# Performance work log

Hardware: AMD Instinct MI355X
Metric: run time of the kernel (lower is better)

Reference implementation:

```python
import jax, jax.numpy as jnp
import numpy as np
from jax import lax


def setup_inputs() -> dict:
    key = jax.random.key(0)
    k1, k2, k3, k4 = jax.random.split(key, 4)
    N, D, B, R, EF = 100000, 256, 64, 32, 32
    storage = jax.random.normal(k1, (N, D), dtype=jnp.float32)
    query = jax.random.normal(k2, (B, D), dtype=jnp.float32)
    graph = jax.random.randint(k3, (N, R), 0, N, dtype=jnp.int32)      # fixed-degree NSW adjacency
    initial = jax.random.randint(k4, (B, EF), 0, N, dtype=jnp.int32)   # random entry points (entry())
    return {"query": query, "storage": storage, "graph": graph,
            "initial": initial, "k": 10, "ef_search": EF}


def reference(query, storage, graph, initial, k, ef_search):
    """Batched greedy best-first NSW search (ef_search fixed expansion steps)."""
    N = storage.shape[0]
    INF = jnp.float32(1e30)

    def sqdist(q, ids):
        diff = storage[ids] - q            # [R, D] gather
        return jnp.sum(diff * diff, axis=-1)

    def search_one(q, init):
        cd = sqdist(q, init)                               # candidate distances [EF]
        visited = jnp.zeros((N,), jnp.bool_).at[init].set(True)
        expanded = jnp.zeros((N,), jnp.bool_)

        def step(state, _):
            cid, cd, visited, expanded = state
            # pick closest unexpanded candidate
            pickd = jnp.where(expanded[cid], INF, cd)
            j = jnp.argmin(pickd)
            u = cid[j]
            expanded = expanded.at[u].set(True)
            # expand neighbors of u
            nbrs = graph[u]                                # [R]
            fresh = ~visited[nbrs]
            nd = jnp.where(fresh, sqdist(q, nbrs), INF)    # skip already-visited
            visited = visited.at[nbrs].set(True)
            # merge candidate pool, keep ef_search best
            all_ids = jnp.concatenate([cid, nbrs])
            all_d = jnp.concatenate([cd, nd])
            negd, idx = lax.top_k(-all_d, ef_search)
            return (all_ids[idx], -negd, visited, expanded), None

        (cid, cd, _, _), _ = lax.scan(step, (init, cd, visited, expanded),
                                      None, length=ef_search)
        negk, idx = lax.top_k(-cd, k)
        return cid[idx], -negk

    topk_ids, topk_dists = jax.vmap(search_one)(query, initial)
    return topk_ids, topk_dists
```

## Files before the change

kernel.cpp:

```cpp
#include <hip/hip_runtime.h>


#define DIMS   256
#define RDEG   32
#define EFPOOL 32
#define KOUT   10
#define NWORDS 3125
#define INF_D  1e30f

__global__ __launch_bounds__(64, 1) void nsw_wave_kernel(
    const float* __restrict__ query,
    const float* __restrict__ storage,
    const int*   __restrict__ graph,
    const int*   __restrict__ initial,
    float*       __restrict__ out,
    int B)
{
    __shared__ unsigned int visited[NWORDS];
    __shared__ unsigned int expanded[NWORDS];
    __shared__ float4 qsh[DIMS / 4];
    __shared__ unsigned long long keys[64];
    __shared__ float sc_d[EFPOOL];
    __shared__ int   sc_id[EFPOOL];

    const int l    = threadIdx.x;
    const int b    = blockIdx.x;
    const int nb   = l & 31;
    const int half = l >> 5;

    for (int i = l; i < NWORDS; i += 64) { visited[i] = 0u; expanded[i] = 0u; }

    qsh[l] = reinterpret_cast<const float4*>(query + (size_t)b * DIMS)[l];

    float pool_d  = INF_D;
    int   pool_id = 0;
    int   u;

    auto merge_pick = [&](float nd, int nbid) {
        float ed  = half ? nd   : pool_d;
        int   eid = half ? nbid : pool_id;
        unsigned long long key =
            ((unsigned long long)__float_as_uint(ed) << 6) | (unsigned)l;
        keys[l] = key;
        int rank = 0;
        #pragma unroll
        for (int j = 0; j < 64; ++j)
            rank += (keys[j] < key) ? 1 : 0;
        if (rank < EFPOOL) { sc_d[rank] = ed; sc_id[rank] = eid; }
        pool_d  = sc_d[nb];
        pool_id = sc_id[nb];
        bool unexp = !((expanded[pool_id >> 5] >> (pool_id & 31)) & 1u);
        unsigned long long m = __ballot(unexp && (l < 32));
        int slot = (m == 0ull) ? 0 : (__ffsll((unsigned long long)m) - 1);
        u = sc_id[slot];
        if (l == 0) expanded[u >> 5] |= (1u << (u & 31));
    };

    {
        int nbid = initial[b * EFPOOL + nb];
        const float4* sp = reinterpret_cast<const float4*>(storage + (size_t)nbid * DIMS) + half * 32;
        float4 r[32];
        #pragma unroll
        for (int j = 0; j < 32; ++j) r[j] = sp[j];
        if (l < 32) atomicOr(&visited[nbid >> 5], 1u << (nbid & 31));
        float a0 = 0.f, a1 = 0.f, a2 = 0.f, a3 = 0.f;
        #pragma unroll
        for (int j = 0; j < 32; ++j) {
            float4 q = qsh[half * 32 + j];
            float d0 = r[j].x - q.x; a0 = fmaf(d0, d0, a0);
            float d1 = r[j].y - q.y; a1 = fmaf(d1, d1, a1);
            float d2 = r[j].z - q.z; a2 = fmaf(d2, d2, a2);
            float d3 = r[j].w - q.w; a3 = fmaf(d3, d3, a3);
        }
        float part = (a0 + a1) + (a2 + a3);
        float nd = part + __shfl_xor(part, 32, 64);
        merge_pick(nd, nbid);
    }

    for (int step = 0; step < EFPOOL; ++step) {
        int nbid = graph[(size_t)u * RDEG + nb];
        const float4* sp = reinterpret_cast<const float4*>(storage + (size_t)nbid * DIMS) + half * 32;
        float4 r[32];
        #pragma unroll
        for (int j = 0; j < 32; ++j) r[j] = sp[j];

        unsigned vw = visited[nbid >> 5];
        bool fresh = !((vw >> (nbid & 31)) & 1u);
        if ((l < 32) && fresh) atomicOr(&visited[nbid >> 5], 1u << (nbid & 31));

        float a0 = 0.f, a1 = 0.f, a2 = 0.f, a3 = 0.f;
        #pragma unroll
        for (int j = 0; j < 32; ++j) {
            float4 q = qsh[half * 32 + j];
            float d0 = r[j].x - q.x; a0 = fmaf(d0, d0, a0);
            float d1 = r[j].y - q.y; a1 = fmaf(d1, d1, a1);
            float d2 = r[j].z - q.z; a2 = fmaf(d2, d2, a2);
            float d3 = r[j].w - q.w; a3 = fmaf(d3, d3, a3);
        }
        float part = (a0 + a1) + (a2 + a3);
        float d = part + __shfl_xor(part, 32, 64);
        float nd = fresh ? d : INF_D;

        merge_pick(nd, nbid);
    }

    if (l < KOUT) {
        out[b * KOUT + l]            = (float)pool_id;
        out[B * KOUT + b * KOUT + l] = pool_d;
    }
}

extern "C" void kernel_launch(void* const* d_in, const int* in_sizes, int n_in,
                              void* d_out, int out_size, void* d_ws, size_t ws_size,
                              hipStream_t stream) {
    const float* query   = (const float*)d_in[0];
    const float* storage = (const float*)d_in[1];
    const int*   graph   = (const int*)d_in[2];
    const int*   initial = (const int*)d_in[3];
    float* out = (float*)d_out;

    const int B = in_sizes[0] / DIMS;

    nsw_wave_kernel<<<B, 64, 0, stream>>>(query, storage, graph, initial, out, B);
}
```

Measured before the change: 235.0 us.

## Transpose distance gather so each lane loads one float4 slice of every neighbor row

The distance computation is reorganized. Before, each lane streamed half of one neighbor's row with strided per-lane loads. Now each lane loads the same float4 column of all 32 neighbor rows, so every wavefront load reads one fully contiguous 1 KB row. The query slice stays in a register instead of LDS, and the 32 partial sums are combined with a shuffle-based transpose reduction. The chosen expansion node is also made wave-uniform with readfirstlane. In exchange the kernel issues many more cross-lane shuffles and must broadcast each neighbor id.

```diff
diff --git a/kernel.cpp b/kernel.cpp
--- a/kernel.cpp
+++ b/kernel.cpp
@@ -18,7 +18,6 @@
 {
     __shared__ unsigned int visited[NWORDS];
     __shared__ unsigned int expanded[NWORDS];
-    __shared__ float4 qsh[DIMS / 4];
     __shared__ unsigned long long keys[64];
     __shared__ float sc_d[EFPOOL];
     __shared__ int   sc_id[EFPOOL];
@@ -30,11 +29,41 @@
 
     for (int i = l; i < NWORDS; i += 64) { visited[i] = 0u; expanded[i] = 0u; }
 
-    qsh[l] = reinterpret_cast<const float4*>(query + (size_t)b * DIMS)[l];
+    const float4 q = reinterpret_cast<const float4*>(query + (size_t)b * DIMS)[l];
 
     float pool_d  = INF_D;
     int   pool_id = 0;
-    int   u;
+    int   u = 0;
+
+    auto dist32 = [&](int nbid) -> float {
+        float4 r[32];
+        #pragma unroll
+        for (int j = 0; j < 32; ++j) {
+            int idj = __shfl(nbid, j, 64);
+            r[j] = reinterpret_cast<const float4*>(storage + (size_t)idj * DIMS)[l];
+        }
+        float w[32];
+        #pragma unroll
+        for (int j = 0; j < 32; ++j) {
+            float d0 = r[j].x - q.x; float a = d0 * d0;
+            float d1 = r[j].y - q.y; a = fmaf(d1, d1, a);
+            float d2 = r[j].z - q.z; a = fmaf(d2, d2, a);
+            float d3 = r[j].w - q.w; a = fmaf(d3, d3, a);
+            w[j] = a;
+        }
+        #pragma unroll
+        for (int k = 0; k < 5; ++k) {
+            const int m  = 1 << k;
+            const int lb = (l >> k) & 1;
+            #pragma unroll
+            for (int i = 0; i < (16 >> k); ++i) {
+                float mine  = w[2 * i + lb];
+                float other = w[2 * i + (1 - lb)];
+                w[i] = mine + __shfl_xor(other, m, 64);
+            }
+        }
+        return w[0] + __shfl_xor(w[0], 32, 64);
+    };
 
     auto merge_pick = [&](float nd, int nbid) {
         float ed  = half ? nd   : pool_d;
@@ -51,56 +80,28 @@
         pool_id = sc_id[nb];
         bool unexp = !((expanded[pool_id >> 5] >> (pool_id & 31)) & 1u);
         unsigned long long m = __ballot(unexp && (l < 32));
-        int slot = (m == 0ull) ? 0 : (__ffsll((unsigned long long)m) - 1);
-        u = sc_id[slot];
+        int slot = (m == 0ull) ? 0 : (__ffsll(m) - 1);
+        u = __builtin_amdgcn_readfirstlane(sc_id[slot]);
         if (l == 0) expanded[u >> 5] |= (1u << (u & 31));
     };
 
     {
         int nbid = initial[b * EFPOOL + nb];
-        const float4* sp = reinterpret_cast<const float4*>(storage + (size_t)nbid * DIMS) + half * 32;
-        float4 r[32];
-        #pragma unroll
-        for (int j = 0; j < 32; ++j) r[j] = sp[j];
         if (l < 32) atomicOr(&visited[nbid >> 5], 1u << (nbid & 31));
-        float a0 = 0.f, a1 = 0.f, a2 = 0.f, a3 = 0.f;
-        #pragma unroll
-        for (int j = 0; j < 32; ++j) {
-            float4 q = qsh[half * 32 + j];
-            float d0 = r[j].x - q.x; a0 = fmaf(d0, d0, a0);
-            float d1 = r[j].y - q.y; a1 = fmaf(d1, d1, a1);
-            float d2 = r[j].z - q.z; a2 = fmaf(d2, d2, a2);
-            float d3 = r[j].w - q.w; a3 = fmaf(d3, d3, a3);
-        }
-        float part = (a0 + a1) + (a2 + a3);
-        float nd = part + __shfl_xor(part, 32, 64);
+        float nd = dist32(nbid);
         merge_pick(nd, nbid);
     }
 
     for (int step = 0; step < EFPOOL; ++step) {
         int nbid = graph[(size_t)u * RDEG + nb];
-        const float4* sp = reinterpret_cast<const float4*>(storage + (size_t)nbid * DIMS) + half * 32;
-        float4 r[32];
-        #pragma unroll
-        for (int j = 0; j < 32; ++j) r[j] = sp[j];
+
+        float d = dist32(nbid);
 
         unsigned vw = visited[nbid >> 5];
         bool fresh = !((vw >> (nbid & 31)) & 1u);
         if ((l < 32) && fresh) atomicOr(&visited[nbid >> 5], 1u << (nbid & 31));
 
-        float a0 = 0.f, a1 = 0.f, a2 = 0.f, a3 = 0.f;
-        #pragma unroll
-        for (int j = 0; j < 32; ++j) {
-            float4 q = qsh[half * 32 + j];
-            float d0 = r[j].x - q.x; a0 = fmaf(d0, d0, a0);
-            float d1 = r[j].y - q.y; a1 = fmaf(d1, d1, a1);
-            float d2 = r[j].z - q.z; a2 = fmaf(d2, d2, a2);
-            float d3 = r[j].w - q.w; a3 = fmaf(d3, d3, a3);
-        }
-        float part = (a0 + a1) + (a2 + a3);
-        float d = part + __shfl_xor(part, 32, 64);
         float nd = fresh ? d : INF_D;
-
         merge_pick(nd, nbid);
     }
 
```

Result: slower. 675.1 us (+187.2%).
